# Performance work log

Hardware: AMD Instinct MI355X
Metric: run time of the kernel (lower is better)

## Reference

```python
import jax, jax.numpy as jnp
import numpy as np

N = 50000
E = 600000
FEAT = 32
ACT = 8
H = 128
HEADS = 4
C = H // HEADS
L = 3
NEG_SLOPE = 0.2
LN_EPS = 1e-5


def setup_inputs() -> dict:
    key = jax.random.key(0)
    ks = jax.random.split(key, 32)
    s = 0.05
    inp = {
        'x': jax.random.normal(ks[0], (N, FEAT), jnp.float32),
        'action': jax.random.normal(ks[1], (N, ACT), jnp.float32),
        'edge_index': jax.random.randint(ks[2], (2, E), 0, N, jnp.int32),
        # node encoder: Linear(feat+act -> H) + LayerNorm
        'W0': jax.random.normal(ks[3], (FEAT + ACT, H), jnp.float32) * s,
        'b0': jnp.zeros((H,), jnp.float32),
        'ln0_g': jnp.ones((H,), jnp.float32),
        'ln0_b': jnp.zeros((H,), jnp.float32),
        # GAT layers (stacked over L): lin W [L,H,heads*C], att vectors, bias, LayerNorm
        'Wg': jax.random.normal(ks[4], (L, H, HEADS * C), jnp.float32) * s,
        'att_src': jax.random.normal(ks[5], (L, HEADS, C), jnp.float32) * s,
        'att_dst': jax.random.normal(ks[6], (L, HEADS, C), jnp.float32) * s,
        'bg': jnp.zeros((L, HEADS * C), jnp.float32),
        'lng_g': jnp.ones((L, H), jnp.float32),
        'lng_b': jnp.zeros((L, H), jnp.float32),
        # dynamics head
        'Wd1': jax.random.normal(ks[7], (H, H), jnp.float32) * s,
        'bd1': jnp.zeros((H,), jnp.float32),
        'Wd2': jax.random.normal(ks[8], (H, FEAT), jnp.float32) * s,
        'bd2': jnp.zeros((FEAT,), jnp.float32),
        # reward head
        'Wr1': jax.random.normal(ks[9], (H, H // 2), jnp.float32) * s,
        'br1': jnp.zeros((H // 2,), jnp.float32),
        'Wr2': jax.random.normal(ks[10], (H // 2, 1), jnp.float32) * s,
        'br2': jnp.zeros((1,), jnp.float32),
        # constraint head
        'Wc1': jax.random.normal(ks[11], (H, H // 2), jnp.float32) * s,
        'bc1': jnp.zeros((H // 2,), jnp.float32),
        'Wc2': jax.random.normal(ks[12], (H // 2, 1), jnp.float32) * s,
        'bc2': jnp.zeros((1,), jnp.float32),
    }
    return inp


def _layernorm(x, g, b):
    mu = jnp.mean(x, axis=-1, keepdims=True)
    var = jnp.mean(jnp.square(x - mu), axis=-1, keepdims=True)
    return (x - mu) * jax.lax.rsqrt(var + LN_EPS) * g + b


def _gat_layer(h, src, dst, W, a_src, a_dst, bias):
    # PyG GATConv: xp = lin(h) per head; alpha = leaky_relu(a_src.x_j + a_dst.x_i)
    xp = (h @ W).reshape(N, HEADS, C)                    # [N, heads, C]
    s_src = jnp.sum(xp * a_src, axis=-1)                 # [N, heads]
    s_dst = jnp.sum(xp * a_dst, axis=-1)                 # [N, heads]
    alpha = jax.nn.leaky_relu(s_src[src] + s_dst[dst], NEG_SLOPE)  # [E', heads]
    # segment softmax over edges grouped by destination node
    amax = jax.ops.segment_max(alpha, dst, num_segments=N)
    ex = jnp.exp(alpha - amax[dst])
    den = jax.ops.segment_sum(ex, dst, num_segments=N)
    attn = ex / den[dst]                                 # [E', heads]
    msg = xp[src] * attn[..., None]                      # [E', heads, C]
    out = jax.ops.segment_sum(msg.reshape(-1, HEADS * C), dst, num_segments=N)
    return out + bias                                    # [N, H]


def reference(x, action, edge_index, W0, b0, ln0_g, ln0_b, Wg, att_src, att_dst,
              bg, lng_g, lng_b, Wd1, bd1, Wd2, bd2, Wr1, br1, Wr2, br2,
              Wc1, bc1, Wc2, bc2):
    # add self loops (PyG GATConv default)
    loops = jnp.arange(N, dtype=edge_index.dtype)
    src = jnp.concatenate([edge_index[0], loops])
    dst = jnp.concatenate([edge_index[1], loops])

    h = jax.nn.relu(_layernorm(jnp.concatenate([x, action], axis=-1) @ W0 + b0, ln0_g, ln0_b))
    for l in range(L):
        h_new = _gat_layer(h, src, dst, Wg[l], att_src[l], att_dst[l], bg[l])
        h_new = jax.nn.relu(_layernorm(h_new, lng_g[l], lng_b[l]))
        h = h + h_new

    delta_x = jax.nn.relu(h @ Wd1 + bd1) @ Wd2 + bd2
    next_x = x + delta_x
    graph_emb = jnp.mean(h, axis=0, keepdims=True)       # global_mean_pool, single graph
    reward = (jax.nn.relu(graph_emb @ Wr1 + br1) @ Wr2 + br2).squeeze(-1)
    constraint_prob = jax.nn.sigmoid(jax.nn.relu(graph_emb @ Wc1 + bc1) @ Wc2 + bc2).squeeze(-1)
    return delta_x, next_x, reward, constraint_prob
```

## Files before the change

### kernel.cpp

```cpp
#include <hip/hip_runtime.h>

typedef unsigned short u16;
typedef __attribute__((ext_vector_type(8))) short bf16x8;
typedef __attribute__((ext_vector_type(4))) float f32x4;

#define NN 50000
#define EE 600000
#define EP 650000
#define LNEPS 1e-5f
#define NB 196
#define ENCB 1563
#define CNTB 2540

__device__ __forceinline__ float bf2f(u16 u) {
    union { unsigned int i; float f; } v; v.i = ((unsigned int)u) << 16; return v.f;
}
__device__ __forceinline__ u16 f2bf(float f) {
    union { float f; unsigned int i; } v; v.f = f;
    unsigned int x = v.i;
    unsigned int r = x + 0x7fffu + ((x >> 16) & 1u);
    return (u16)(r >> 16);
}
__device__ __forceinline__ float ldf(const void* p, long i, int bf) {
    return bf ? bf2f(((const u16*)p)[i]) : ((const float*)p)[i];
}
__device__ __forceinline__ void stf(void* p, long i, int bf, float v) {
    if (bf) ((u16*)p)[i] = f2bf(v); else ((float*)p)[i] = v;
}

#define WTOT 93858
#define BSWN 65536
struct P22 { const void* p[22]; };

__global__ __launch_bounds__(256) void init7(P22 w, float* __restrict__ wf,
                                             u16* __restrict__ bsw,
                                             int* __restrict__ deg,
                                             float* __restrict__ gacc,
                                             int* __restrict__ flag) {
    const unsigned w0 = *(const unsigned*)w.p[2];
    const int bf = (w0 == 0x3F803F80u) ? 1 : 0;
    int i = blockIdx.x * 256 + threadIdx.x;
    if (i < WTOT) {
        const int offs[23] = {0,5120,5248,5376,5504,54656,55040,55424,55808,56192,56576,
                              72960,73088,77184,77216,85408,85472,85536,85537,93729,93793,
                              93857,93858};
        int seg = 0;
        while (offs[seg + 1] <= i) ++seg;
        wf[i] = ldf(w.p[seg], i - offs[seg], bf);
        return;
    }
    i -= WTOT;
    if (i < BSWN) {
        int mat = i >> 14, rem = i & 16383;
        int ct = rem >> 11, r2 = rem & 2047;
        int kb = r2 >> 9, r3 = r2 & 511;
        int lane = r3 >> 3, j = r3 & 7;
        int k = kb * 32 + (lane >> 4) * 8 + j;
        int n = ct * 16 + (lane & 15);
        float v = (mat < 3) ? ldf(w.p[4], (long)mat * 16384 + (long)k * 128 + n, bf)
                            : ldf(w.p[10], (long)k * 128 + n, bf);
        bsw[i] = f2bf(v);
        return;
    }
    i -= BSWN;
    if (i < NN) { deg[i] = 0; return; }
    i -= NN;
    if (i < 2048) { gacc[i] = 0.f; return; }
    if (i == 2048) *flag = bf;
}

__global__ __launch_bounds__(256) void enc8(
    const void* __restrict__ x, const void* __restrict__ act,
    const float* __restrict__ wf, u16* __restrict__ hb,
    const int* __restrict__ flg, const int* __restrict__ ei,
    int* __restrict__ deg, int* __restrict__ rank) {
    if (blockIdx.x >= ENCB) {
        int e = (blockIdx.x - ENCB) * 256 + threadIdx.x;
        if (e < EP) {
            int d = (e < EE) ? ei[EE + e] : (e - EE);
            rank[e] = atomicAdd(&deg[d], 1);
        }
        return;
    }
    const float* W0f = wf;
    const float* b0f = wf + 5120;
    const float* gf  = wf + 5248;
    const float* bbf = wf + 5376;
    __shared__ float As[32][41];
    const int bf = *flg;
    int t = threadIdx.x;
    int r0 = blockIdx.x * 32;
    #pragma unroll
    for (int i = 0; i < 5; ++i) {
        int idx = t + i * 256;
        int r = idx / 40, k = idx - r * 40;
        int rr = r0 + r; if (rr >= NN) rr = NN - 1;
        As[r][k] = (k < 32) ? ldf(x, (long)rr * 32 + k, bf)
                            : ldf(act, (long)rr * 8 + (k - 32), bf);
    }
    __syncthreads();
    int colq = t & 31, mq = t >> 5;
    int col0 = colq * 4;
    float4 b0v = *(const float4*)(b0f + col0);
    float acc[4][4];
    #pragma unroll
    for (int j = 0; j < 4; ++j) {
        acc[j][0] = b0v.x; acc[j][1] = b0v.y; acc[j][2] = b0v.z; acc[j][3] = b0v.w;
    }
    #pragma unroll 2
    for (int k = 0; k < 40; ++k) {
        float4 b4 = *(const float4*)(W0f + k * 128 + col0);
        float a0 = As[mq * 4 + 0][k];
        float a1 = As[mq * 4 + 1][k];
        float a2 = As[mq * 4 + 2][k];
        float a3 = As[mq * 4 + 3][k];
        acc[0][0] += a0 * b4.x; acc[0][1] += a0 * b4.y; acc[0][2] += a0 * b4.z; acc[0][3] += a0 * b4.w;
        acc[1][0] += a1 * b4.x; acc[1][1] += a1 * b4.y; acc[1][2] += a1 * b4.z; acc[1][3] += a1 * b4.w;
        acc[2][0] += a2 * b4.x; acc[2][1] += a2 * b4.y; acc[2][2] += a2 * b4.z; acc[2][3] += a2 * b4.w;
        acc[3][0] += a3 * b4.x; acc[3][1] += a3 * b4.y; acc[3][2] += a3 * b4.z; acc[3][3] += a3 * b4.w;
    }
    float4 gv = *(const float4*)(gf + col0);
    float4 bv = *(const float4*)(bbf + col0);
    #pragma unroll
    for (int j = 0; j < 4; ++j) {
        int row = r0 + mq * 4 + j;
        float pa = acc[j][0] + acc[j][1] + acc[j][2] + acc[j][3];
        #pragma unroll
        for (int o = 1; o <= 16; o <<= 1) pa += __shfl_xor(pa, o, 32);
        float mu = pa * (1.f / 128.f);
        float d0 = acc[j][0] - mu, d1 = acc[j][1] - mu;
        float d2 = acc[j][2] - mu, d3 = acc[j][3] - mu;
        float q = d0 * d0 + d1 * d1 + d2 * d2 + d3 * d3;
        #pragma unroll
        for (int o = 1; o <= 16; o <<= 1) q += __shfl_xor(q, o, 32);
        float rs = rsqrtf(q * (1.f / 128.f) + LNEPS);
        if (row < NN) {
            ushort4 hbv;
            hbv.x = f2bf(fmaxf(d0 * rs * gv.x + bv.x, 0.f));
            hbv.y = f2bf(fmaxf(d1 * rs * gv.y + bv.y, 0.f));
            hbv.z = f2bf(fmaxf(d2 * rs * gv.z + bv.z, 0.f));
            hbv.w = f2bf(fmaxf(d3 * rs * gv.w + bv.w, 0.f));
            *(ushort4*)(hb + (long)row * 128 + col0) = hbv;
        }
    }
}

__global__ __launch_bounds__(256) void lin9(
    const u16* __restrict__ hb, const u16* __restrict__ bswm,
    const float* __restrict__ bias, u16* __restrict__ out, int dorelu,
    int doscore, const float* __restrict__ wf, int layer,
    float* __restrict__ s_src, float* __restrict__ s_dst,
    int douth, const void* __restrict__ x, void* __restrict__ dout,
    const int* __restrict__ flg,
    int doscatter, const int* __restrict__ ei, const int* __restrict__ rank,
    const int* __restrict__ offs, int* __restrict__ csrc,
    float* __restrict__ gacc) {
    if (doscatter && blockIdx.x >= ENCB) {
        int e = (blockIdx.x - ENCB) * 256 + threadIdx.x;
        if (e < EP) {
            int s, d;
            if (e < EE) { s = ei[e]; d = ei[EE + e]; } else { s = e - EE; d = s; }
            csrc[offs[d] + rank[e]] = s;
        }
        return;
    }
    __shared__ u16 As[32 * 136];
    __shared__ u16 ts[32 * 136];
    __shared__ float ps[128];
    int t = threadIdx.x;
    int r0 = blockIdx.x * 32;
    #pragma unroll
    for (int i = 0; i < 2; ++i) {
        int idx = (t + i * 256) * 8;
        int r = idx >> 7, k = idx & 127;
        int rr = r0 + r; if (rr >= NN) rr = NN - 1;
        int4 v = *(const int4*)(hb + (long)rr * 128 + k);
        *(int4*)(As + r * 136 + k) = v;
    }
    __syncthreads();
    int w = t >> 6, lane = t & 63;
    int rt = w & 1, ctbase = (w >> 1) * 4;
    int quad = lane >> 4, l15 = lane & 15;
    int rowl = rt * 16 + l15;
    bf16x8 afr[4];
    #pragma unroll
    for (int kb = 0; kb < 4; ++kb)
        afr[kb] = *(const bf16x8*)(As + rowl * 136 + kb * 32 + quad * 8);
    const float* asrf = wf + 54656 + layer * 128;
    const float* adsf = wf + 55040 + layer * 128;
    int headbase = (w >> 1) * 2;
    #pragma unroll
    for (int cp = 0; cp < 2; ++cp) {
        int ct0 = ctbase + cp * 2, ct1 = ct0 + 1;
        f32x4 acc0 = {0.f, 0.f, 0.f, 0.f};
        f32x4 acc1 = {0.f, 0.f, 0.f, 0.f};
        #pragma unroll
        for (int kb = 0; kb < 4; ++kb) {
            bf16x8 b0 = *(const bf16x8*)(bswm + ct0 * 2048 + kb * 512 + lane * 8);
            acc0 = __builtin_amdgcn_mfma_f32_16x16x32_bf16(afr[kb], b0, acc0, 0, 0, 0);
        }
        #pragma unroll
// ... 44 lines not shown
        __syncthreads();
        const float* Wd2f = wf + 73088;
        const float* bd2f = wf + 77184;
        const int bf = *flg;
        int c = t & 31, mq = t >> 5;
        float acc[4];
        #pragma unroll
        for (int j = 0; j < 4; ++j) acc[j] = bd2f[c];
        #pragma unroll 4
        for (int k = 0; k < 128; ++k) {
            float wv = Wd2f[k * 32 + c];
            acc[0] += bf2f(ts[(mq * 4 + 0) * 136 + k]) * wv;
            acc[1] += bf2f(ts[(mq * 4 + 1) * 136 + k]) * wv;
            acc[2] += bf2f(ts[(mq * 4 + 2) * 136 + k]) * wv;
            acc[3] += bf2f(ts[(mq * 4 + 3) * 136 + k]) * wv;
        }
        #pragma unroll
        for (int j = 0; j < 4; ++j) {
            int node = r0 + mq * 4 + j;
            if (node >= NN) continue;
            stf(dout, (long)node * 32 + c, bf, acc[j]);
            stf(dout, (long)NN * 32 + (long)node * 32 + c, bf,
                ldf(x, (long)node * 32 + c, bf) + acc[j]);
        }
        int pc = t & 127, half = t >> 7;
        float s = 0.f;
        #pragma unroll
        for (int r2 = half * 16; r2 < half * 16 + 16; ++r2) {
            if (r0 + r2 < NN) s += bf2f(As[r2 * 136 + pc]);
        }
        if (half == 0) ps[pc] = s;
        __syncthreads();
        if (half == 1) atomicAdd(&gacc[(blockIdx.x & 15) * 128 + pc], s + ps[pc]);
    }
}

__global__ __launch_bounds__(256) void scanA(const int* __restrict__ deg,
                                             int* __restrict__ bsum) {
    __shared__ int red[256];
    int t = threadIdx.x; int i = blockIdx.x * 256 + t;
    red[t] = (i < NN) ? deg[i] : 0; __syncthreads();
    for (int s = 128; s >= 1; s >>= 1) { if (t < s) red[t] += red[t + s]; __syncthreads(); }
    if (t == 0) bsum[blockIdx.x] = red[0];
}

__global__ __launch_bounds__(256) void scanC3(const int* __restrict__ deg,
                                              const int* __restrict__ bsum,
                                              int* __restrict__ offs) {
    __shared__ int sh[256];
    int t = threadIdx.x;
    sh[t] = (t < NB) ? bsum[t] : 0;
    __syncthreads();
    for (int o = 1; o < 256; o <<= 1) {
        int u = (t >= o) ? sh[t - o] : 0;
        __syncthreads();
        sh[t] += u;
        __syncthreads();
    }
    int pre = (blockIdx.x == 0) ? 0 : sh[blockIdx.x - 1];
    __syncthreads();
    int i = blockIdx.x * 256 + t;
    int v = (i < NN) ? deg[i] : 0;
    sh[t] = v;
    __syncthreads();
    for (int o = 1; o < 256; o <<= 1) {
        int u = (t >= o) ? sh[t - o] : 0;
        __syncthreads();
        sh[t] += u;
        __syncthreads();
    }
    if (i < NN) offs[i] = pre + sh[t] - v;
    if (i == 0) offs[NN] = EP;
}

__global__ __launch_bounds__(256) void agg10(
    const u16* __restrict__ xp, const float* __restrict__ s_src,
    const float* __restrict__ s_dst,
    const int* __restrict__ csrc, const int* __restrict__ offs,
    const float* __restrict__ wf, int layer, u16* __restrict__ hb) {
    const float* bgf = wf + 55424 + layer * 128;
    const float* gf  = wf + 55808 + layer * 128;
    const float* bbf = wf + 56192 + layer * 128;
    int t = threadIdx.x;
    int lane = t & 63;
    int n = blockIdx.x * 4 + (t >> 6);
    int q = (lane >> 4) & 3;
    int l16 = lane & 15;
    int c0 = l16 * 8;
    int hd = l16 >> 2;
    long idx0 = (long)n * 128 + c0;
    int4 hold = *(const int4*)(hb + idx0);
    float sdn = s_dst[n * 4 + (lane & 3)];
    int beg = offs[n], end = offs[n + 1];
    float a[8] = {};
    float den = 0.f;
    for (int cbeg = beg; cbeg < end; cbeg += 64) {
        int cdeg = end - cbeg; if (cdeg > 64) cdeg = 64;
        int eidx = (lane < cdeg) ? csrc[cbeg + lane] : n;
        for (int base = 0; base < cdeg; base += 16) {
            int me = base + (lane >> 2);
            int sm = __shfl(eidx, me & 63, 64);
            float aw = s_src[sm * 4 + (lane & 3)] + sdn;
            aw = (aw > 0.f) ? aw : 0.2f * aw;
            float wv = (me < cdeg) ? __expf(aw) : 0.f;
            int s00 = __shfl(eidx, base + q, 64);
// ... 31 lines not shown
    v[0] = a[0] * inv + bg0.x; v[1] = a[1] * inv + bg0.y;
    v[2] = a[2] * inv + bg0.z; v[3] = a[3] * inv + bg0.w;
    v[4] = a[4] * inv + bg1.x; v[5] = a[5] * inv + bg1.y;
    v[6] = a[6] * inv + bg1.z; v[7] = a[7] * inv + bg1.w;
    float pa = v[0] + v[1] + v[2] + v[3] + v[4] + v[5] + v[6] + v[7];
    #pragma unroll
    for (int o = 1; o <= 8; o <<= 1) pa += __shfl_xor(pa, o, 16);
    float mu = pa * (1.f / 128.f);
    float d[8];
    float qv = 0.f;
    #pragma unroll
    for (int k = 0; k < 8; ++k) { d[k] = v[k] - mu; qv += d[k] * d[k]; }
    #pragma unroll
    for (int o = 1; o <= 8; o <<= 1) qv += __shfl_xor(qv, o, 16);
    float rs = rsqrtf(qv * (1.f / 128.f) + LNEPS);
    float4 g0 = *(const float4*)(gf + c0);
    float4 g1 = *(const float4*)(gf + c0 + 4);
    float4 b0 = *(const float4*)(bbf + c0);
    float4 b1 = *(const float4*)(bbf + c0 + 4);
    float gg[8]  = {g0.x, g0.y, g0.z, g0.w, g1.x, g1.y, g1.z, g1.w};
    float bbv[8] = {b0.x, b0.y, b0.z, b0.w, b1.x, b1.y, b1.z, b1.w};
    if (lane < 16) {
        union { int4 i; u16 u[8]; } hv, ho;
        ho.i = hold;
        #pragma unroll
        for (int k = 0; k < 8; ++k) {
            float y = fmaxf(d[k] * rs * gg[k] + bbv[k], 0.f);
            hv.u[k] = f2bf(bf2f(ho.u[k]) + y);
        }
        *(int4*)(hb + idx0) = hv.i;
    }
}

__global__ __launch_bounds__(128) void head5(
    const float* __restrict__ gacc, const float* __restrict__ wf,
    void* __restrict__ out, const int* __restrict__ flg) {
    const float* Wr1f = wf + 77216;
    const float* br1f = wf + 85408;
    const float* Wr2f = wf + 85472;
    const float* br2f = wf + 85536;
    const float* Wc1f = wf + 85537;
    const float* bc1f = wf + 93729;
    const float* Wc2f = wf + 93793;
    const float* bc2f = wf + 93857;
    __shared__ float ge[128];
    __shared__ float hr[128];
    const int bf = *flg;
    int t = threadIdx.x;
    {
        float s = 0.f;
        #pragma unroll
        for (int k2 = 0; k2 < 16; ++k2) s += gacc[k2 * 128 + t];
        ge[t] = s * (1.f / (float)NN);
    }
    __syncthreads();
    {
        int j = t & 63;
        const float* W = (t < 64) ? Wr1f : Wc1f;
        const float* bb = (t < 64) ? br1f : bc1f;
        float a = bb[j];
        for (int k = 0; k < 128; ++k) a += ge[k] * W[k * 64 + j];
        hr[t] = fmaxf(a, 0.f);
    }
    __syncthreads();
    if (t == 0) {
        float r = br2f[0];
        for (int j = 0; j < 64; ++j) r += hr[j] * Wr2f[j];
        stf(out, (long)2 * NN * 32, bf, r);
    } else if (t == 1) {
        float z = bc2f[0];
        for (int j = 0; j < 64; ++j) z += hr[64 + j] * Wc2f[j];
        float p = 1.f / (1.f + __expf(-z));
        stf(out, (long)2 * NN * 32 + 1, bf, p);
    }
}

extern "C" void kernel_launch(void* const* d_in, const int* in_sizes, int n_in,
                              void* d_out, int out_size, void* d_ws, size_t ws_size,
                              hipStream_t stream) {
    const void* x   = d_in[0];
    const void* act = d_in[1];
    const int*  ei  = (const int*)d_in[2];

    char* ws = (char*)d_ws;
    size_t off = 0;
    auto alloc = [&](size_t bytes) -> char* {
        char* p = ws + off;
        off = (off + bytes + 255) & ~(size_t)255;
        return p;
    };
    u16*       hb     = (u16*)      alloc((size_t)NN * 128 * 2);
    u16*       xp     = (u16*)      alloc((size_t)NN * 128 * 2);
    float*     s_src  = (float*)    alloc((size_t)NN * 4 * 4);
    float*     s_dst  = (float*)    alloc((size_t)NN * 4 * 4);
    int*       deg    = (int*)      alloc((size_t)NN * 4);
    int*       rank   = (int*)      alloc((size_t)EP * 4);
    int*       offs   = (int*)      alloc((size_t)(NN + 1) * 4);
    int*       csrc   = (int*)      alloc((size_t)EP * 4);
    float*     wf     = (float*)    alloc((size_t)WTOT * 4);
    u16*       bsw    = (u16*)      alloc((size_t)BSWN * 2);
    float*     gacc   = (float*)    alloc(16 * 128 * 4);
    int*       flag   = (int*)      alloc(4);
    int*       bsum   = (int*)      alloc((size_t)NB * 4);

    P22 wp;
    for (int i = 0; i < 22; ++i) wp.p[i] = d_in[3 + i];
    const int initN = WTOT + BSWN + NN + 2048 + 1;
    init7<<<(initN + 255) / 256, 256, 0, stream>>>(wp, wf, bsw, deg, gacc, flag);

    enc8<<<ENCB + CNTB, 256, 0, stream>>>(x, act, wf, hb, flag, ei, deg, rank);

    scanA<<<NB, 256, 0, stream>>>(deg, bsum);
    scanC3<<<NB, 256, 0, stream>>>(deg, bsum, offs);

    for (int l = 0; l < 3; ++l) {
        int grid = (l == 0) ? (ENCB + CNTB) : ENCB;
        lin9<<<grid, 256, 0, stream>>>(hb, bsw + (size_t)l * 16384,
                                       (const float*)nullptr, xp, 0,
                                       1, wf, l, s_src, s_dst,
                                       0, x, d_out, flag,
                                       (l == 0) ? 1 : 0, ei, rank, offs, csrc, gacc);
        agg10<<<NN / 4, 256, 0, stream>>>(xp, s_src, s_dst, csrc, offs,
                                          wf, l, hb);
    }

    lin9<<<ENCB, 256, 0, stream>>>(hb, bsw + (size_t)3 * 16384,
                                   wf + 72960, xp, 1,
                                   0, wf, 0, s_src, s_dst,
                                   1, x, d_out, flag,
                                   0, ei, rank, offs, csrc, gacc);

    head5<<<1, 128, 0, stream>>>(gacc, wf, d_out, flag);

    (void)in_sizes; (void)n_in; (void)out_size; (void)ws_size;
}
```

Baseline: 350.9 us.

## Fuse encoder, degree count, scan and CSR scatter into one spin-synced kernel

Merges the node encoder, in-degree counting, the two-pass prefix scan and the CSR scatter into a single launch. Scan blocks spin-wait on global counters for the count blocks and for each other. Degree atomics are spread over 8 replicas per node to cut contention. The encoder now reads raw weights directly instead of the prepacked fp32 copy, and the head kernel is folded into the last block of the final linear via a completion counter. This removes several launches and serial scan passes, but it relies on all scan blocks being co-resident and adds spin-wait and fence overhead.

```diff
diff --git a/kernel.cpp b/kernel.cpp
--- a/kernel.cpp
+++ b/kernel.cpp
@@ -10,7 +10,7 @@
 #define LNEPS 1e-5f
 #define NB 196
 #define ENCB 1563
-#define CNTB 2540
+#define HB 2344
 
 __device__ __forceinline__ float bf2f(u16 u) {
     union { unsigned int i; float f; } v; v.i = ((unsigned int)u) << 16; return v.f;
@@ -32,10 +32,11 @@
 #define BSWN 65536
 struct P22 { const void* p[22]; };
 
-__global__ __launch_bounds__(256) void init7(P22 w, float* __restrict__ wf,
+__global__ __launch_bounds__(256) void init8(P22 w, float* __restrict__ wf,
                                              u16* __restrict__ bsw,
-                                             int* __restrict__ deg,
+                                             int* __restrict__ deg8,
                                              float* __restrict__ gacc,
+                                             int* __restrict__ ctrs,
                                              int* __restrict__ flag) {
     const unsigned w0 = *(const unsigned*)w.p[2];
     const int bf = (w0 == 0x3F803F80u) ? 1 : 0;
@@ -63,110 +64,194 @@
         return;
     }
     i -= BSWN;
-    if (i < NN) { deg[i] = 0; return; }
-    i -= NN;
+    if (i < NN * 8) { deg8[i] = 0; return; }
+    i -= NN * 8;
     if (i < 2048) { gacc[i] = 0.f; return; }
-    if (i == 2048) *flag = bf;
-}
-
-__global__ __launch_bounds__(256) void enc8(
+    i -= 2048;
+    if (i < 4) { ctrs[i] = 0; return; }
+    if (i == 4) *flag = bf;
+}
+
+__global__ __launch_bounds__(256) void mega2(
     const void* __restrict__ x, const void* __restrict__ act,
-    const float* __restrict__ wf, u16* __restrict__ hb,
-    const int* __restrict__ flg, const int* __restrict__ ei,
-    int* __restrict__ deg, int* __restrict__ rank) {
-    if (blockIdx.x >= ENCB) {
-        int e = (blockIdx.x - ENCB) * 256 + threadIdx.x;
-        if (e < EP) {
-            int d = (e < EE) ? ei[EE + e] : (e - EE);
-            rank[e] = atomicAdd(&deg[d], 1);
+    const int* __restrict__ ei,
+    const void* __restrict__ W0p, const void* __restrict__ b0p,
+    const void* __restrict__ g0p, const void* __restrict__ bb0p,
+    u16* __restrict__ hb,
+    int* __restrict__ deg8, int* __restrict__ rank,
+    int* __restrict__ bsum, int* __restrict__ offs,
+    int* __restrict__ repOff8, int* __restrict__ csrc,
+    int* __restrict__ ctrs) {
+    int b = blockIdx.x, t = threadIdx.x;
+    if (b < ENCB) {
+        const int bf = (*(const unsigned*)g0p == 0x3F803F80u) ? 1 : 0;
+        __shared__ float As[32][41];
+        int r0 = b * 32;
+        #pragma unroll
+        for (int i = 0; i < 5; ++i) {
+            int idx = t + i * 256;
+            int r = idx / 40, k = idx - r * 40;
+            int rr = r0 + r; if (rr >= NN) rr = NN - 1;
+            As[r][k] = (k < 32) ? ldf(x, (long)rr * 32 + k, bf)
+                                : ldf(act, (long)rr * 8 + (k - 32), bf);
+        }
+        __syncthreads();
+        int colq = t & 31, mq = t >> 5;
+        int col0 = colq * 4;
+        float acc[4][4];
+        {
+            float b0 = ldf(b0p, col0, bf), b1 = ldf(b0p, col0 + 1, bf);
+            float b2 = ldf(b0p, col0 + 2, bf), b3 = ldf(b0p, col0 + 3, bf);
+            #pragma unroll
+            for (int j = 0; j < 4; ++j) {
+                acc[j][0] = b0; acc[j][1] = b1; acc[j][2] = b2; acc[j][3] = b3;
+            }
+        }
+        #pragma unroll 2
+        for (int k = 0; k < 40; ++k) {
+            float w0 = ldf(W0p, (long)k * 128 + col0, bf);
+            float w1 = ldf(W0p, (long)k * 128 + col0 + 1, bf);
+            float w2 = ldf(W0p, (long)k * 128 + col0 + 2, bf);
+            float w3 = ldf(W0p, (long)k * 128 + col0 + 3, bf);
+            float a0 = As[mq * 4 + 0][k];
+            float a1 = As[mq * 4 + 1][k];
+            float a2 = As[mq * 4 + 2][k];
+            float a3 = As[mq * 4 + 3][k];
+            acc[0][0] += a0 * w0; acc[0][1] += a0 * w1; acc[0][2] += a0 * w2; acc[0][3] += a0 * w3;
+            acc[1][0] += a1 * w0; acc[1][1] += a1 * w1; acc[1][2] += a1 * w2; acc[1][3] += a1 * w3;
+            acc[2][0] += a2 * w0; acc[2][1] += a2 * w1; acc[2][2] += a2 * w2; acc[2][3] += a2 * w3;
+            acc[3][0] += a3 * w0; acc[3][1] += a3 * w1; acc[3][2] += a3 * w2; acc[3][3] += a3 * w3;
+        }
+        float gv0 = ldf(g0p, col0, bf), gv1 = ldf(g0p, col0 + 1, bf);
+        float gv2 = ldf(g0p, col0 + 2, bf), gv3 = ldf(g0p, col0 + 3, bf);
+        float bv0 = ldf(bb0p, col0, bf), bv1 = ldf(bb0p, col0 + 1, bf);
+        float bv2 = ldf(bb0p, col0 + 2, bf), bv3 = ldf(bb0p, col0 + 3, bf);
+        #pragma unroll
+        for (int j = 0; j < 4; ++j) {
+            int row = r0 + mq * 4 + j;
+            float pa = acc[j][0] + acc[j][1] + acc[j][2] + acc[j][3];
+            #pragma unroll
+            for (int o = 1; o <= 16; o <<= 1) pa += __shfl_xor(pa, o, 32);
+            float mu = pa * (1.f / 128.f);
+            float d0 = acc[j][0] - mu, d1 = acc[j][1] - mu;
+            float d2 = acc[j][2] - mu, d3 = acc[j][3] - mu;
+            float q = d0 * d0 + d1 * d1 + d2 * d2 + d3 * d3;
+            #pragma unroll
+            for (int o = 1; o <= 16; o <<= 1) q += __shfl_xor(q, o, 32);
+            float rs = rsqrtf(q * (1.f / 128.f) + LNEPS);
+            if (row < NN) {
+                ushort4 hbv;
+                hbv.x = f2bf(fmaxf(d0 * rs * gv0 + bv0, 0.f));
+                hbv.y = f2bf(fmaxf(d1 * rs * gv1 + bv1, 0.f));
+                hbv.z = f2bf(fmaxf(d2 * rs * gv2 + bv2, 0.f));
+                hbv.w = f2bf(fmaxf(d3 * rs * gv3 + bv3, 0.f));
+                *(ushort4*)(hb + (long)row * 128 + col0) = hbv;
+            }
         }
         return;
     }
-    const float* W0f = wf;
-    const float* b0f = wf + 5120;
-    const float* gf  = wf + 5248;
-    const float* bbf = wf + 5376;
-    __shared__ float As[32][41];
-    const int bf = *flg;
-    int t = threadIdx.x;
-    int r0 = blockIdx.x * 32;
-    #pragma unroll
-    for (int i = 0; i < 5; ++i) {
-        int idx = t + i * 256;
-        int r = idx / 40, k = idx - r * 40;
-        int rr = r0 + r; if (rr >= NN) rr = NN - 1;
-        As[r][k] = (k < 32) ? ldf(x, (long)rr * 32 + k, bf)
-                            : ldf(act, (long)rr * 8 + (k - 32), bf);
+    b -= ENCB;
+    if (b < HB) {
+        int e = b * 256 + t;
+        if (e < EE) {
+            int d = ei[EE + e];
+            int rep = (e >> 8) & 7;
+            int r = atomicAdd(&deg8[d * 8 + rep], 1);
+            __hip_atomic_store(&rank[e], r, __ATOMIC_RELAXED, __HIP_MEMORY_SCOPE_AGENT);
+        }
+        __syncthreads();
+        if (t == 0) { __threadfence(); atomicAdd(&ctrs[0], 1); }
+        return;
+    }
+    b -= HB;
+    __shared__ int sh[256];
+    if (t == 0) {
+        while (__hip_atomic_load(&ctrs[0], __ATOMIC_ACQUIRE, __HIP_MEMORY_SCOPE_AGENT) < HB)
+            __builtin_amdgcn_s_sleep(2);
     }
     __syncthreads();
-    int colq = t & 31, mq = t >> 5;
-    int col0 = colq * 4;
-    float4 b0v = *(const float4*)(b0f + col0);
-    float acc[4][4];
-    #pragma unroll
-    for (int j = 0; j < 4; ++j) {
-        acc[j][0] = b0v.x; acc[j][1] = b0v.y; acc[j][2] = b0v.z; acc[j][3] = b0v.w;
-    }
-    #pragma unroll 2
-    for (int k = 0; k < 40; ++k) {
-        float4 b4 = *(const float4*)(W0f + k * 128 + col0);
-        float a0 = As[mq * 4 + 0][k];
-        float a1 = As[mq * 4 + 1][k];
-        float a2 = As[mq * 4 + 2][k];
-        float a3 = As[mq * 4 + 3][k];
-        acc[0][0] += a0 * b4.x; acc[0][1] += a0 * b4.y; acc[0][2] += a0 * b4.z; acc[0][3] += a0 * b4.w;
-        acc[1][0] += a1 * b4.x; acc[1][1] += a1 * b4.y; acc[1][2] += a1 * b4.z; acc[1][3] += a1 * b4.w;
-        acc[2][0] += a2 * b4.x; acc[2][1] += a2 * b4.y; acc[2][2] += a2 * b4.z; acc[2][3] += a2 * b4.w;
-        acc[3][0] += a3 * b4.x; acc[3][1] += a3 * b4.y; acc[3][2] += a3 * b4.z; acc[3][3] += a3 * b4.w;
-    }
-    float4 gv = *(const float4*)(gf + col0);
-    float4 bv = *(const float4*)(bbf + col0);
-    #pragma unroll
-    for (int j = 0; j < 4; ++j) {
-        int row = r0 + mq * 4 + j;
-        float pa = acc[j][0] + acc[j][1] + acc[j][2] + acc[j][3];
-        #pragma unroll
-        for (int o = 1; o <= 16; o <<= 1) pa += __shfl_xor(pa, o, 32);
-        float mu = pa * (1.f / 128.f);
-        float d0 = acc[j][0] - mu, d1 = acc[j][1] - mu;
-        float d2 = acc[j][2] - mu, d3 = acc[j][3] - mu;
-        float q = d0 * d0 + d1 * d1 + d2 * d2 + d3 * d3;
-        #pragma unroll
-        for (int o = 1; o <= 16; o <<= 1) q += __shfl_xor(q, o, 32);
-        float rs = rsqrtf(q * (1.f / 128.f) + LNEPS);
-        if (row < NN) {
-            ushort4 hbv;
-            hbv.x = f2bf(fmaxf(d0 * rs * gv.x + bv.x, 0.f));
-            hbv.y = f2bf(fmaxf(d1 * rs * gv.y + bv.y, 0.f));
-            hbv.z = f2bf(fmaxf(d2 * rs * gv.z + bv.z, 0.f));
-            hbv.w = f2bf(fmaxf(d3 * rs * gv.w + bv.w, 0.f));
-            *(ushort4*)(hb + (long)row * 128 + col0) = hbv;
-        }
-    }
-}
-
-__global__ __launch_bounds__(256) void lin9(
+    __threadfence();
+    int i = b * 256 + t;
+    int c[8]; int s = 0;
+    if (i < NN) {
+        int4 lo = *(const int4*)(deg8 + (long)i * 8);
+        int4 hi = *(const int4*)(deg8 + (long)i * 8 + 4);
+        c[0] = lo.x; c[1] = lo.y; c[2] = lo.z; c[3] = lo.w;
+        c[4] = hi.x; c[5] = hi.y; c[6] = hi.z; c[7] = hi.w;
+        s = c[0] + c[1] + c[2] + c[3] + c[4] + c[5] + c[6] + c[7] + 1;
+    }
+    sh[t] = s; __syncthreads();
+    for (int o = 1; o < 256; o <<= 1) {
+        int u = (t >= o) ? sh[t - o] : 0;
+        __syncthreads(); sh[t] += u; __syncthreads();
+    }
+    int total = sh[255];
+    int localinc = sh[t];
+    if (t == 0)
+        __hip_atomic_store(&bsum[b], total, __ATOMIC_RELAXED, __HIP_MEMORY_SCOPE_AGENT);
+    __syncthreads();
+    if (t == 0) {
+        __threadfence();
+        atomicAdd(&ctrs[1], 1);
+        while (__hip_atomic_load(&ctrs[1], __ATOMIC_ACQUIRE, __HIP_MEMORY_SCOPE_AGENT) < NB)
+            __builtin_amdgcn_s_sleep(2);
+    }
+    __syncthreads();
+    int bv = (t < NB) ? __hip_atomic_load(&bsum[t], __ATOMIC_RELAXED, __HIP_MEMORY_SCOPE_AGENT) : 0;
+    sh[t] = bv; __syncthreads();
+    for (int o = 1; o < 256; o <<= 1) {
+        int u = (t >= o) ? sh[t - o] : 0;
+        __syncthreads(); sh[t] += u; __syncthreads();
+    }
+    int pre = (b == 0) ? 0 : sh[b - 1];
+    __syncthreads();
+    if (i < NN) {
+        int excl = pre + localinc - s;
+        offs[i] = excl;
+        int rp[8]; int run = 0;
+        #pragma unroll
+        for (int r2 = 0; r2 < 8; ++r2) { rp[r2] = run; run += c[r2]; }
+        int4 v0; v0.x = rp[0]; v0.y = rp[1]; v0.z = rp[2]; v0.w = rp[3];
+        int4 v1; v1.x = rp[4]; v1.y = rp[5]; v1.z = rp[6]; v1.w = rp[7];
+        *(int4*)(repOff8 + (long)i * 8) = v0;
+        *(int4*)(repOff8 + (long)i * 8 + 4) = v1;
+        if (i == NN - 1) offs[NN] = EP;
+    }
+    if (t == 0) {
+        __threadfence();
+        atomicAdd(&ctrs[2], 1);
+        while (__hip_atomic_load(&ctrs[2], __ATOMIC_ACQUIRE, __HIP_MEMORY_SCOPE_AGENT) < NB)
+            __builtin_amdgcn_s_sleep(2);
+    }
+    __syncthreads();
+    __threadfence();
+    for (int e = b * 256 + t; e < EP; e += NB * 256) {
+        if (e < EE) {
+            int sv = ei[e], d = ei[EE + e];
+            int rep = (e >> 8) & 7;
+            int r = __hip_atomic_load(&rank[e], __ATOMIC_RELAXED, __HIP_MEMORY_SCOPE_AGENT);
+            csrc[offs[d] + repOff8[(long)d * 8 + rep] + r] = sv;
+        } else {
+            int n = e - EE;
+            csrc[offs[n + 1] - 1] = n;
+        }
+    }
+}
+
+__global__ __launch_bounds__(256) void lin10(
     const u16* __restrict__ hb, const u16* __restrict__ bswm,
     const float* __restrict__ bias, u16* __restrict__ out, int dorelu,
     int doscore, const float* __restrict__ wf, int layer,
     float* __restrict__ s_src, float* __restrict__ s_dst,
     int douth, const void* __restrict__ x, void* __restrict__ dout,
-    const int* __restrict__ flg,
-    int doscatter, const int* __restrict__ ei, const int* __restrict__ rank,
-    const int* __restrict__ offs, int* __restrict__ csrc,
-    float* __restrict__ gacc) {
-    if (doscatter && blockIdx.x >= ENCB) {
-        int e = (blockIdx.x - ENCB) * 256 + threadIdx.x;
-        if (e < EP) {
-            int s, d;
-            if (e < EE) { s = ei[e]; d = ei[EE + e]; } else { s = e - EE; d = s; }
-            csrc[offs[d] + rank[e]] = s;
-        }
-        return;
-    }
+    const int* __restrict__ flg, float* __restrict__ gacc,
+    int* __restrict__ ctrs) {
     __shared__ u16 As[32 * 136];
     __shared__ u16 ts[32 * 136];
     __shared__ float ps[128];
+    __shared__ float ge[128];
+    __shared__ float hr[128];
+    __shared__ int lastb;
     int t = threadIdx.x;
     int r0 = blockIdx.x * 32;
     #pragma unroll
@@ -277,45 +362,53 @@
         if (half == 0) ps[pc] = s;
         __syncthreads();
         if (half == 1) atomicAdd(&gacc[(blockIdx.x & 15) * 128 + pc], s + ps[pc]);
-    }
-}
-
-__global__ __launch_bounds__(256) void scanA(const int* __restrict__ deg,
-                                             int* __restrict__ bsum) {
-    __shared__ int red[256];
-    int t = threadIdx.x; int i = blockIdx.x * 256 + t;
-    red[t] = (i < NN) ? deg[i] : 0; __syncthreads();
-    for (int s = 128; s >= 1; s >>= 1) { if (t < s) red[t] += red[t + s]; __syncthreads(); }
-    if (t == 0) bsum[blockIdx.x] = red[0];
-}
-
-__global__ __launch_bounds__(256) void scanC3(const int* __restrict__ deg,
-                                              const int* __restrict__ bsum,
-                                              int* __restrict__ offs) {
-    __shared__ int sh[256];
-    int t = threadIdx.x;
-    sh[t] = (t < NB) ? bsum[t] : 0;
-    __syncthreads();
-    for (int o = 1; o < 256; o <<= 1) {
-        int u = (t >= o) ? sh[t - o] : 0;
         __syncthreads();
-        sh[t] += u;
+        if (t == 0) {
+            __threadfence();
+            int p = atomicAdd(&ctrs[3], 1);
+            lastb = (p == ENCB - 1);
+        }
         __syncthreads();
-    }
-    int pre = (blockIdx.x == 0) ? 0 : sh[blockIdx.x - 1];
-    __syncthreads();
-    int i = blockIdx.x * 256 + t;
-    int v = (i < NN) ? deg[i] : 0;
-    sh[t] = v;
-    __syncthreads();
-    for (int o = 1; o < 256; o <<= 1) {
-        int u = (t >= o) ? sh[t - o] : 0;
-        __syncthreads();
-        sh[t] += u;
-        __syncthreads();
-    }
-    if (i < NN) offs[i] = pre + sh[t] - v;
-    if (i == 0) offs[NN] = EP;
+        if (lastb) {
+            __threadfence();
+            const float* Wr1f = wf + 77216;
+            const float* br1f = wf + 85408;
+            const float* Wr2f = wf + 85472;
+            const float* br2f = wf + 85536;
+            const float* Wc1f = wf + 85537;
+            const float* bc1f = wf + 93729;
+            const float* Wc2f = wf + 93793;
+            const float* bc2f = wf + 93857;
+            if (t < 128) {
+                float s2 = 0.f;
+                #pragma unroll
+                for (int k2 = 0; k2 < 16; ++k2)
+                    s2 += __hip_atomic_load(&gacc[k2 * 128 + t], __ATOMIC_RELAXED,
+                                            __HIP_MEMORY_SCOPE_AGENT);
+                ge[t] = s2 * (1.f / (float)NN);
+            }
+            __syncthreads();
+            if (t < 128) {
+                int j = t & 63;
+                const float* W = (t < 64) ? Wr1f : Wc1f;
+                const float* bb = (t < 64) ? br1f : bc1f;
+                float a = bb[j];
+                for (int k = 0; k < 128; ++k) a += ge[k] * W[k * 64 + j];
+                hr[t] = fmaxf(a, 0.f);
+            }
+            __syncthreads();
+            if (t == 0) {
+                float r = br2f[0];
+                for (int j = 0; j < 64; ++j) r += hr[j] * Wr2f[j];
+                stf(dout, (long)2 * NN * 32, bf, r);
+            } else if (t == 1) {
+                float z = bc2f[0];
+                for (int j = 0; j < 64; ++j) z += hr[64 + j] * Wc2f[j];
+                float p2 = 1.f / (1.f + __expf(-z));
+                stf(dout, (long)2 * NN * 32 + 1, bf, p2);
+            }
+        }
+    }
 }
 
 __global__ __launch_bounds__(256) void agg10(
@@ -413,49 +506,6 @@
     }
 }
 
-__global__ __launch_bounds__(128) void head5(
-    const float* __restrict__ gacc, const float* __restrict__ wf,
-    void* __restrict__ out, const int* __restrict__ flg) {
-    const float* Wr1f = wf + 77216;
-    const float* br1f = wf + 85408;
-    const float* Wr2f = wf + 85472;
-    const float* br2f = wf + 85536;
-    const float* Wc1f = wf + 85537;
-    const float* bc1f = wf + 93729;
-    const float* Wc2f = wf + 93793;
-    const float* bc2f = wf + 93857;
-    __shared__ float ge[128];
-    __shared__ float hr[128];
-    const int bf = *flg;
-    int t = threadIdx.x;
-    {
-        float s = 0.f;
-        #pragma unroll
-        for (int k2 = 0; k2 < 16; ++k2) s += gacc[k2 * 128 + t];
-        ge[t] = s * (1.f / (float)NN);
-    }
-    __syncthreads();
-    {
-        int j = t & 63;
-        const float* W = (t < 64) ? Wr1f : Wc1f;
-        const float* bb = (t < 64) ? br1f : bc1f;
-        float a = bb[j];
-        for (int k = 0; k < 128; ++k) a += ge[k] * W[k * 64 + j];
-        hr[t] = fmaxf(a, 0.f);
-    }
-    __syncthreads();
-    if (t == 0) {
-        float r = br2f[0];
-        for (int j = 0; j < 64; ++j) r += hr[j] * Wr2f[j];
-        stf(out, (long)2 * NN * 32, bf, r);
-    } else if (t == 1) {
-        float z = bc2f[0];
-        for (int j = 0; j < 64; ++j) z += hr[64 + j] * Wc2f[j];
-        float p = 1.f / (1.f + __expf(-z));
-        stf(out, (long)2 * NN * 32 + 1, bf, p);
-    }
-}
-
 extern "C" void kernel_launch(void* const* d_in, const int* in_sizes, int n_in,
                               void* d_out, int out_size, void* d_ws, size_t ws_size,
                               hipStream_t stream) {
@@ -470,48 +520,44 @@
         off = (off + bytes + 255) & ~(size_t)255;
         return p;
     };
-    u16*       hb     = (u16*)      alloc((size_t)NN * 128 * 2);
-    u16*       xp     = (u16*)      alloc((size_t)NN * 128 * 2);
-    float*     s_src  = (float*)    alloc((size_t)NN * 4 * 4);
-    float*     s_dst  = (float*)    alloc((size_t)NN * 4 * 4);
-    int*       deg    = (int*)      alloc((size_t)NN * 4);
-    int*       rank   = (int*)      alloc((size_t)EP * 4);
-    int*       offs   = (int*)      alloc((size_t)(NN + 1) * 4);
-    int*       csrc   = (int*)      alloc((size_t)EP * 4);
-    float*     wf     = (float*)    alloc((size_t)WTOT * 4);
-    u16*       bsw    = (u16*)      alloc((size_t)BSWN * 2);
-    float*     gacc   = (float*)    alloc(16 * 128 * 4);
-    int*       flag   = (int*)      alloc(4);
-    int*       bsum   = (int*)      alloc((size_t)NB * 4);
+    u16*       hb      = (u16*)   alloc((size_t)NN * 128 * 2);
+    u16*       xp      = (u16*)   alloc((size_t)NN * 128 * 2);
+    float*     s_src   = (float*) alloc((size_t)NN * 4 * 4);
+    float*     s_dst   = (float*) alloc((size_t)NN * 4 * 4);
+    int*       deg8    = (int*)   alloc((size_t)NN * 8 * 4);
+    int*       rank    = (int*)   alloc((size_t)EE * 4);
+    int*       offs    = (int*)   alloc((size_t)(NN + 1) * 4);
+    int*       repOff8 = (int*)   alloc((size_t)NN * 8 * 4);
+    int*       csrc    = (int*)   alloc((size_t)EP * 4);
+    float*     wf      = (float*) alloc((size_t)WTOT * 4);
+    u16*       bsw     = (u16*)   alloc((size_t)BSWN * 2);
+    float*     gacc    = (float*) alloc(16 * 128 * 4);
+    int*       ctrs    = (int*)   alloc(4 * 4);
+    int*       flag    = (int*)   alloc(4);
+    int*       bsum    = (int*)   alloc((size_t)NB * 4);
 
     P22 wp;
     for (int i = 0; i < 22; ++i) wp.p[i] = d_in[3 + i];
-    const int initN = WTOT + BSWN + NN + 2048 + 1;
-    init7<<<(initN + 255) / 256, 256, 0, stream>>>(wp, wf, bsw, deg, gacc, flag);
-
-    enc8<<<ENCB + CNTB, 256, 0, stream>>>(x, act, wf, hb, flag, ei, deg, rank);
-
-    scanA<<<NB, 256, 0, stream>>>(deg, bsum);
-    scanC3<<<NB, 256, 0, stream>>>(deg, bsum, offs);
+    const int initN = WTOT + BSWN + NN * 8 + 2048 + 4 + 1;
+    init8<<<(initN + 255) / 256, 256, 0, stream>>>(wp, wf, bsw, deg8, gacc, ctrs, flag);
+
+    mega2<<<ENCB + HB + NB, 256, 0, stream>>>(
+        x, act, ei, d_in[3], d_in[4], d_in[5], d_in[6],
+        hb, deg8, rank, bsum, offs, repOff8, csrc, ctrs);
 
     for (int l = 0; l < 3; ++l) {
-        int grid = (l == 0) ? (ENCB + CNTB) : ENCB;
-        lin9<<<grid, 256, 0, stream>>>(hb, bsw + (size_t)l * 16384,
-                                       (const float*)nullptr, xp, 0,
-                                       1, wf, l, s_src, s_dst,
-                                       0, x, d_out, flag,
-                                       (l == 0) ? 1 : 0, ei, rank, offs, csrc, gacc);
+        lin10<<<ENCB, 256, 0, stream>>>(hb, bsw + (size_t)l * 16384,
+                                        (const float*)nullptr, xp, 0,
+                                        1, wf, l, s_src, s_dst,
+                                        0, x, d_out, flag, gacc, ctrs);
         agg10<<<NN / 4, 256, 0, stream>>>(xp, s_src, s_dst, csrc, offs,
                                           wf, l, hb);
     }
 
-    lin9<<<ENCB, 256, 0, stream>>>(hb, bsw + (size_t)3 * 16384,
-                                   wf + 72960, xp, 1,
-                                   0, wf, 0, s_src, s_dst,
-                                   1, x, d_out, flag,
-                                   0, ei, rank, offs, csrc, gacc);
-
-    head5<<<1, 128, 0, stream>>>(gacc, wf, d_out, flag);
+    lin10<<<ENCB, 256, 0, stream>>>(hb, bsw + (size_t)3 * 16384,
+                                    wf + 72960, xp, 1,
+                                    0, wf, 0, s_src, s_dst,
+                                    1, x, d_out, flag, gacc, ctrs);
 
     (void)in_sizes; (void)n_in; (void)out_size; (void)ws_size;
 }
```

New measurement: 622.4 us. +77.4%, slower.

## Replicate degree counters eightfold and fold head into last block

Applied to the files above, without the earlier changes.

Degree counting now spreads atomics over 8 replicated counters per destination node, picked by block index, to reduce atomic contention on hot nodes. Self-loops are no longer counted with atomics; they are placed analytically at the end of each node's CSR segment. The scan computes per-replica offsets so the scatter can place edges correctly. The separate head kernel is removed and its work runs in the last-finishing block of the final linear kernel, chosen with an atomic counter and thread fences. The costs are more scan memory traffic, an extra offset array, and a serial tail on the last block.

```diff
diff --git a/kernel.cpp b/kernel.cpp
--- a/kernel.cpp
+++ b/kernel.cpp
@@ -10,6 +10,7 @@
 #define LNEPS 1e-5f
 #define NB 196
 #define ENCB 1563
+#define HB 2344
 #define CNTB 2540
 
 __device__ __forceinline__ float bf2f(u16 u) {
@@ -32,10 +33,11 @@
 #define BSWN 65536
 struct P22 { const void* p[22]; };
 
-__global__ __launch_bounds__(256) void init7(P22 w, float* __restrict__ wf,
+__global__ __launch_bounds__(256) void init8(P22 w, float* __restrict__ wf,
                                              u16* __restrict__ bsw,
-                                             int* __restrict__ deg,
+                                             int* __restrict__ deg8,
                                              float* __restrict__ gacc,
+                                             int* __restrict__ ctrs,
                                              int* __restrict__ flag) {
     const unsigned w0 = *(const unsigned*)w.p[2];
     const int bf = (w0 == 0x3F803F80u) ? 1 : 0;
@@ -63,22 +65,26 @@
         return;
     }
     i -= BSWN;
-    if (i < NN) { deg[i] = 0; return; }
-    i -= NN;
+    if (i < NN * 8) { deg8[i] = 0; return; }
+    i -= NN * 8;
     if (i < 2048) { gacc[i] = 0.f; return; }
-    if (i == 2048) *flag = bf;
-}
-
-__global__ __launch_bounds__(256) void enc8(
+    i -= 2048;
+    if (i < 4) { ctrs[i] = 0; return; }
+    if (i == 4) *flag = bf;
+}
+
+__global__ __launch_bounds__(256) void enc9(
     const void* __restrict__ x, const void* __restrict__ act,
     const float* __restrict__ wf, u16* __restrict__ hb,
     const int* __restrict__ flg, const int* __restrict__ ei,
-    int* __restrict__ deg, int* __restrict__ rank) {
+    int* __restrict__ deg8, int* __restrict__ rank) {
     if (blockIdx.x >= ENCB) {
-        int e = (blockIdx.x - ENCB) * 256 + threadIdx.x;
-        if (e < EP) {
-            int d = (e < EE) ? ei[EE + e] : (e - EE);
-            rank[e] = atomicAdd(&deg[d], 1);
+        int hbk = blockIdx.x - ENCB;
+        int e = hbk * 256 + threadIdx.x;
+        if (e < EE) {
+            int d = ei[EE + e];
+            int rep = hbk & 7;
+            rank[e] = atomicAdd(&deg8[d * 8 + rep], 1);
         }
         return;
     }
@@ -145,7 +151,68 @@
     }
 }
 
-__global__ __launch_bounds__(256) void lin9(
+__global__ __launch_bounds__(256) void scanA2(const int* __restrict__ deg8,
+                                              int* __restrict__ bsum) {
+    __shared__ int red[256];
+    int t = threadIdx.x; int i = blockIdx.x * 256 + t;
+    int s = 0;
+    if (i < NN) {
+        int4 lo = *(const int4*)(deg8 + (long)i * 8);
+        int4 hi = *(const int4*)(deg8 + (long)i * 8 + 4);
+        s = lo.x + lo.y + lo.z + lo.w + hi.x + hi.y + hi.z + hi.w + 1;
+    }
+    red[t] = s; __syncthreads();
+    for (int s2 = 128; s2 >= 1; s2 >>= 1) { if (t < s2) red[t] += red[t + s2]; __syncthreads(); }
+    if (t == 0) bsum[blockIdx.x] = red[0];
+}
+
+__global__ __launch_bounds__(256) void scanC4(const int* __restrict__ deg8,
+                                              const int* __restrict__ bsum,
+                                              int* __restrict__ offs,
+                                              int* __restrict__ repOff8) {
+    __shared__ int sh[256];
+    int t = threadIdx.x;
+    sh[t] = (t < NB) ? bsum[t] : 0;
+    __syncthreads();
+    for (int o = 1; o < 256; o <<= 1) {
+        int u = (t >= o) ? sh[t - o] : 0;
+        __syncthreads();
+        sh[t] += u;
+        __syncthreads();
+    }
+    int pre = (blockIdx.x == 0) ? 0 : sh[blockIdx.x - 1];
+    __syncthreads();
+    int i = blockIdx.x * 256 + t;
+    int c[8]; int v = 0;
+    if (i < NN) {
+        int4 lo = *(const int4*)(deg8 + (long)i * 8);
+        int4 hi = *(const int4*)(deg8 + (long)i * 8 + 4);
+        c[0] = lo.x; c[1] = lo.y; c[2] = lo.z; c[3] = lo.w;
+        c[4] = hi.x; c[5] = hi.y; c[6] = hi.z; c[7] = hi.w;
+        v = c[0] + c[1] + c[2] + c[3] + c[4] + c[5] + c[6] + c[7] + 1;
+    }
+    sh[t] = v;
+    __syncthreads();
+    for (int o = 1; o < 256; o <<= 1) {
+        int u = (t >= o) ? sh[t - o] : 0;
+        __syncthreads();
+        sh[t] += u;
+        __syncthreads();
+    }
+    if (i < NN) {
+        offs[i] = pre + sh[t] - v;
+        int rp[8]; int run = 0;
+        #pragma unroll
+        for (int r2 = 0; r2 < 8; ++r2) { rp[r2] = run; run += c[r2]; }
+        int4 v0; v0.x = rp[0]; v0.y = rp[1]; v0.z = rp[2]; v0.w = rp[3];
+        int4 v1; v1.x = rp[4]; v1.y = rp[5]; v1.z = rp[6]; v1.w = rp[7];
+        *(int4*)(repOff8 + (long)i * 8) = v0;
+        *(int4*)(repOff8 + (long)i * 8 + 4) = v1;
+    }
+    if (i == 0) offs[NN] = EP;
+}
+
+__global__ __launch_bounds__(256) void lin11(
     const u16* __restrict__ hb, const u16* __restrict__ bswm,
     const float* __restrict__ bias, u16* __restrict__ out, int dorelu,
     int doscore, const float* __restrict__ wf, int layer,
@@ -153,20 +220,28 @@
     int douth, const void* __restrict__ x, void* __restrict__ dout,
     const int* __restrict__ flg,
     int doscatter, const int* __restrict__ ei, const int* __restrict__ rank,
-    const int* __restrict__ offs, int* __restrict__ csrc,
-    float* __restrict__ gacc) {
+    const int* __restrict__ offs, const int* __restrict__ repOff8,
+    int* __restrict__ csrc, float* __restrict__ gacc, int* __restrict__ ctrs) {
     if (doscatter && blockIdx.x >= ENCB) {
         int e = (blockIdx.x - ENCB) * 256 + threadIdx.x;
         if (e < EP) {
-            int s, d;
-            if (e < EE) { s = ei[e]; d = ei[EE + e]; } else { s = e - EE; d = s; }
-            csrc[offs[d] + rank[e]] = s;
+            if (e < EE) {
+                int sv = ei[e], d = ei[EE + e];
+                int rep = (e >> 8) & 7;
+                csrc[offs[d] + repOff8[(long)d * 8 + rep] + rank[e]] = sv;
+            } else {
+                int n = e - EE;
+                csrc[offs[n + 1] - 1] = n;
+            }
         }
         return;
     }
     __shared__ u16 As[32 * 136];
     __shared__ u16 ts[32 * 136];
     __shared__ float ps[128];
+    __shared__ float ge[128];
+    __shared__ float hr[128];
+    __shared__ int lastb;
     int t = threadIdx.x;
     int r0 = blockIdx.x * 32;
     #pragma unroll
@@ -277,45 +352,53 @@
         if (half == 0) ps[pc] = s;
         __syncthreads();
         if (half == 1) atomicAdd(&gacc[(blockIdx.x & 15) * 128 + pc], s + ps[pc]);
-    }
-}
-
-__global__ __launch_bounds__(256) void scanA(const int* __restrict__ deg,
-                                             int* __restrict__ bsum) {
-    __shared__ int red[256];
-    int t = threadIdx.x; int i = blockIdx.x * 256 + t;
-    red[t] = (i < NN) ? deg[i] : 0; __syncthreads();
-    for (int s = 128; s >= 1; s >>= 1) { if (t < s) red[t] += red[t + s]; __syncthreads(); }
-    if (t == 0) bsum[blockIdx.x] = red[0];
-}
-
-__global__ __launch_bounds__(256) void scanC3(const int* __restrict__ deg,
-                                              const int* __restrict__ bsum,
-                                              int* __restrict__ offs) {
-    __shared__ int sh[256];
-    int t = threadIdx.x;
-    sh[t] = (t < NB) ? bsum[t] : 0;
-    __syncthreads();
-    for (int o = 1; o < 256; o <<= 1) {
-        int u = (t >= o) ? sh[t - o] : 0;
-        __syncthreads();
-        sh[t] += u;
-        __syncthreads();
-    }
-    int pre = (blockIdx.x == 0) ? 0 : sh[blockIdx.x - 1];
-    __syncthreads();
-    int i = blockIdx.x * 256 + t;
-    int v = (i < NN) ? deg[i] : 0;
-    sh[t] = v;
-    __syncthreads();
-    for (int o = 1; o < 256; o <<= 1) {
-        int u = (t >= o) ? sh[t - o] : 0;
-        __syncthreads();
-        sh[t] += u;
-        __syncthreads();
-    }
-    if (i < NN) offs[i] = pre + sh[t] - v;
-    if (i == 0) offs[NN] = EP;
+        __syncthreads();
+        if (t == 0) {
+            __threadfence();
+            int p = atomicAdd(&ctrs[3], 1);
+            lastb = (p == ENCB - 1);
+        }
+        __syncthreads();
+        if (lastb) {
+            __threadfence();
+            const float* Wr1f = wf + 77216;
+            const float* br1f = wf + 85408;
+            const float* Wr2f = wf + 85472;
+            const float* br2f = wf + 85536;
+            const float* Wc1f = wf + 85537;
+            const float* bc1f = wf + 93729;
+            const float* Wc2f = wf + 93793;
+            const float* bc2f = wf + 93857;
+            if (t < 128) {
+                float s2 = 0.f;
+                #pragma unroll
+                for (int k2 = 0; k2 < 16; ++k2)
+                    s2 += __hip_atomic_load(&gacc[k2 * 128 + t], __ATOMIC_RELAXED,
+                                            __HIP_MEMORY_SCOPE_AGENT);
+                ge[t] = s2 * (1.f / (float)NN);
+            }
+            __syncthreads();
+            if (t < 128) {
+                int j = t & 63;
+                const float* W = (t < 64) ? Wr1f : Wc1f;
+                const float* bb = (t < 64) ? br1f : bc1f;
+                float a = bb[j];
+                for (int k = 0; k < 128; ++k) a += ge[k] * W[k * 64 + j];
+                hr[t] = fmaxf(a, 0.f);
+            }
+            __syncthreads();
+            if (t == 0) {
+                float r = br2f[0];
+                for (int j = 0; j < 64; ++j) r += hr[j] * Wr2f[j];
+                stf(dout, (long)2 * NN * 32, bf, r);
+            } else if (t == 1) {
+                float z = bc2f[0];
+                for (int j = 0; j < 64; ++j) z += hr[64 + j] * Wc2f[j];
+                float p2 = 1.f / (1.f + __expf(-z));
+                stf(dout, (long)2 * NN * 32 + 1, bf, p2);
+            }
+        }
+    }
 }
 
 __global__ __launch_bounds__(256) void agg10(
@@ -413,49 +496,6 @@
     }
 }
 
-__global__ __launch_bounds__(128) void head5(
-    const float* __restrict__ gacc, const float* __restrict__ wf,
-    void* __restrict__ out, const int* __restrict__ flg) {
-    const float* Wr1f = wf + 77216;
-    const float* br1f = wf + 85408;
-    const float* Wr2f = wf + 85472;
-    const float* br2f = wf + 85536;
-    const float* Wc1f = wf + 85537;
-    const float* bc1f = wf + 93729;
-    const float* Wc2f = wf + 93793;
-    const float* bc2f = wf + 93857;
-    __shared__ float ge[128];
-    __shared__ float hr[128];
-    const int bf = *flg;
-    int t = threadIdx.x;
-    {
-        float s = 0.f;
-        #pragma unroll
-        for (int k2 = 0; k2 < 16; ++k2) s += gacc[k2 * 128 + t];
-        ge[t] = s * (1.f / (float)NN);
-    }
-    __syncthreads();
-    {
-        int j = t & 63;
-        const float* W = (t < 64) ? Wr1f : Wc1f;
-        const float* bb = (t < 64) ? br1f : bc1f;
-        float a = bb[j];
-        for (int k = 0; k < 128; ++k) a += ge[k] * W[k * 64 + j];
-        hr[t] = fmaxf(a, 0.f);
-    }
-    __syncthreads();
-    if (t == 0) {
-        float r = br2f[0];
-        for (int j = 0; j < 64; ++j) r += hr[j] * Wr2f[j];
-        stf(out, (long)2 * NN * 32, bf, r);
-    } else if (t == 1) {
-        float z = bc2f[0];
-        for (int j = 0; j < 64; ++j) z += hr[64 + j] * Wc2f[j];
-        float p = 1.f / (1.f + __expf(-z));
-        stf(out, (long)2 * NN * 32 + 1, bf, p);
-    }
-}
-
 extern "C" void kernel_launch(void* const* d_in, const int* in_sizes, int n_in,
                               void* d_out, int out_size, void* d_ws, size_t ws_size,
                               hipStream_t stream) {
@@ -470,48 +510,50 @@
         off = (off + bytes + 255) & ~(size_t)255;
         return p;
     };
-    u16*       hb     = (u16*)      alloc((size_t)NN * 128 * 2);
-    u16*       xp     = (u16*)      alloc((size_t)NN * 128 * 2);
-    float*     s_src  = (float*)    alloc((size_t)NN * 4 * 4);
-    float*     s_dst  = (float*)    alloc((size_t)NN * 4 * 4);
-    int*       deg    = (int*)      alloc((size_t)NN * 4);
-    int*       rank   = (int*)      alloc((size_t)EP * 4);
-    int*       offs   = (int*)      alloc((size_t)(NN + 1) * 4);
-    int*       csrc   = (int*)      alloc((size_t)EP * 4);
-    float*     wf     = (float*)    alloc((size_t)WTOT * 4);
-    u16*       bsw    = (u16*)      alloc((size_t)BSWN * 2);
-    float*     gacc   = (float*)    alloc(16 * 128 * 4);
-    int*       flag   = (int*)      alloc(4);
-    int*       bsum   = (int*)      alloc((size_t)NB * 4);
+    u16*       hb      = (u16*)   alloc((size_t)NN * 128 * 2);
+    u16*       xp      = (u16*)   alloc((size_t)NN * 128 * 2);
+    float*     s_src   = (float*) alloc((size_t)NN * 4 * 4);
+    float*     s_dst   = (float*) alloc((size_t)NN * 4 * 4);
+    int*       deg8    = (int*)   alloc((size_t)NN * 8 * 4);
+    int*       rank    = (int*)   alloc((size_t)EE * 4);
+    int*       offs    = (int*)   alloc((size_t)(NN + 1) * 4);
+    int*       repOff8 = (int*)   alloc((size_t)NN * 8 * 4);
+    int*       csrc    = (int*)   alloc((size_t)EP * 4);
+    float*     wf      = (float*) alloc((size_t)WTOT * 4);
+    u16*       bsw     = (u16*)   alloc((size_t)BSWN * 2);
+    float*     gacc    = (float*) alloc(16 * 128 * 4);
+    int*       ctrs    = (int*)   alloc(4 * 4);
+    int*       flag    = (int*)   alloc(4);
+    int*       bsum    = (int*)   alloc((size_t)NB * 4);
 
     P22 wp;
     for (int i = 0; i < 22; ++i) wp.p[i] = d_in[3 + i];
-    const int initN = WTOT + BSWN + NN + 2048 + 1;
-    init7<<<(initN + 255) / 256, 256, 0, stream>>>(wp, wf, bsw, deg, gacc, flag);
-
-    enc8<<<ENCB + CNTB, 256, 0, stream>>>(x, act, wf, hb, flag, ei, deg, rank);
-
-    scanA<<<NB, 256, 0, stream>>>(deg, bsum);
-    scanC3<<<NB, 256, 0, stream>>>(deg, bsum, offs);
+    const int initN = WTOT + BSWN + NN * 8 + 2048 + 4 + 1;
+    init8<<<(initN + 255) / 256, 256, 0, stream>>>(wp, wf, bsw, deg8, gacc, ctrs, flag);
+
+    enc9<<<ENCB + HB, 256, 0, stream>>>(x, act, wf, hb, flag, ei, deg8, rank);
+
+    scanA2<<<NB, 256, 0, stream>>>(deg8, bsum);
+    scanC4<<<NB, 256, 0, stream>>>(deg8, bsum, offs, repOff8);
 
     for (int l = 0; l < 3; ++l) {
         int grid = (l == 0) ? (ENCB + CNTB) : ENCB;
-        lin9<<<grid, 256, 0, stream>>>(hb, bsw + (size_t)l * 16384,
-                                       (const float*)nullptr, xp, 0,
-                                       1, wf, l, s_src, s_dst,
-                                       0, x, d_out, flag,
-                                       (l == 0) ? 1 : 0, ei, rank, offs, csrc, gacc);
+        lin11<<<grid, 256, 0, stream>>>(hb, bsw + (size_t)l * 16384,
+                                        (const float*)nullptr, xp, 0,
+                                        1, wf, l, s_src, s_dst,
+                                        0, x, d_out, flag,
+                                        (l == 0) ? 1 : 0, ei, rank, offs, repOff8,
+                                        csrc, gacc, ctrs);
         agg10<<<NN / 4, 256, 0, stream>>>(xp, s_src, s_dst, csrc, offs,
                                           wf, l, hb);
     }
 
-    lin9<<<ENCB, 256, 0, stream>>>(hb, bsw + (size_t)3 * 16384,
-                                   wf + 72960, xp, 1,
-                                   0, wf, 0, s_src, s_dst,
-                                   1, x, d_out, flag,
-                                   0, ei, rank, offs, csrc, gacc);
-
-    head5<<<1, 128, 0, stream>>>(gacc, wf, d_out, flag);
+    lin11<<<ENCB, 256, 0, stream>>>(hb, bsw + (size_t)3 * 16384,
+                                    wf + 72960, xp, 1,
+                                    0, wf, 0, s_src, s_dst,
+                                    1, x, d_out, flag,
+                                    0, ei, rank, offs, repOff8,
+                                    csrc, gacc, ctrs);
 
     (void)in_sizes; (void)n_in; (void)out_size; (void)ws_size;
 }
```

Result: slower. 386.4 us (+10.1%).
